# Optimization experiments

Hardware: AMD Instinct MI355X
Metric: run time of the kernel (lower is better)

## Reference

```python
import jax, jax.numpy as jnp
import numpy as np

B_, L_, DM, DS, DC, EX = 4, 2048, 1024, 16, 4, 2
DI = DM * EX

def setup_inputs() -> dict:
    key = jax.random.key(0)
    ks = jax.random.split(key, 8)
    s = lambda i, shape, scale: jax.random.normal(ks[i], shape, jnp.float32) * scale
    return dict(
        x=s(0, (B_, L_, DM), 1.0),
        in_proj_w=s(1, (2 * DI, DM), 0.02),
        conv_weight=s(2, (DI, DC), 0.1),
        conv_bias=jnp.zeros((DI,), jnp.float32),
        A_log=jax.random.uniform(ks[3], (DS,), jnp.float32, -4.0, -1.0),
        D=jnp.ones((DI,), jnp.float32),
        delta_w=s(4, (DS, DI), 0.02),
        delta_b=jnp.ones((DS,), jnp.float32),
        B_w=s(5, (DS, DI), 0.02),
        C_w=s(6, (DS, DI), 0.02),
        out_proj_w=s(7, (DM, DI), 0.02),
    )

def reference(x, in_proj_w, conv_weight, conv_bias, A_log, D, delta_w, delta_b, B_w, C_w, out_proj_w):
    Bb, L, Dm = x.shape
    di, dc = conv_weight.shape
    # 1. input projection and split into ssm / gate branches
    x_inner = x @ in_proj_w.T                       # [B,L,2*di]
    x_ssm, x_gate = x_inner[..., :di], x_inner[..., di:]
    # 2. causal depthwise conv1d + SiLU (kernel size dc, per-channel weights)
    xp = jnp.pad(x_ssm, ((0, 0), (dc - 1, 0), (0, 0)))
    xc = conv_bias + sum(xp[:, k:k + L, :] * conv_weight[:, k] for k in range(dc))
    x_conv = jax.nn.silu(xc)                         # [B,L,di]
    # 3. content-aware discretization
    delta = jax.nn.softplus(x_conv @ delta_w.T + delta_b)  # [B,L,N]
    Bs = x_conv @ B_w.T                              # [B,L,N]
    Cs = x_conv @ C_w.T                              # [B,L,N]
    A = -jnp.exp(A_log)                              # [N]
    xavg = x_conv.mean(axis=-1)                      # [B,L]
    # 4. selective SSM scan over L with state h:[B,N]
    def step(h, inp):
        dt, bt, ct, xa = inp                         # [B,N],[B,N],[B,N],[B]
        h = jnp.exp(dt * A) * h + dt * bt * xa[:, None]
        return h, (h * ct).sum(-1)                   # y_t: [B]
    h0 = jnp.zeros((Bb, A.shape[0]), x.dtype)
    _, ys = jax.lax.scan(
        step, h0,
        (delta.transpose(1, 0, 2), Bs.transpose(1, 0, 2), Cs.transpose(1, 0, 2), xavg.T))
    y_ssm = ys.T[..., None]                          # [B,L,1] (broadcasts over di)
    # 5. gate, skip, output projection
    y_gated = y_ssm * jax.nn.silu(x_gate)
    y_skip = y_gated + x_conv * D
    return y_skip @ out_proj_w.T                     # [B,L,D]
```

## Files before the change

### kernel.cpp

```cpp
#include <hip/hip_runtime.h>
#include <cmath>

#define LL 2048
#define NROW 8192
#define DMODEL 1024
#define DINNER 2048
#define NSTATE 16
#define NSEG 64
#define SEGLEN 32

typedef unsigned short u16;
typedef __attribute__((ext_vector_type(8))) unsigned short u16x8;
typedef __attribute__((ext_vector_type(8))) short short8;
typedef __attribute__((ext_vector_type(4))) float floatx4;
typedef __attribute__((ext_vector_type(16))) float floatx16;

__device__ __forceinline__ float bf2f(u16 h) {
    unsigned u = ((unsigned)h) << 16;
    float f;
    __builtin_memcpy(&f, &u, 4);
    return f;
}
__device__ __forceinline__ u16 f2bf(float f) {
    unsigned u;
    __builtin_memcpy(&u, &f, 4);
    u = u + 0x7fffu + ((u >> 16) & 1u);
    return (u16)(u >> 16);
}
__device__ __forceinline__ float silu_f(float x) { return x / (1.f + __expf(-x)); }

__global__ __launch_bounds__(256) void cvt_multi(
    const float* __restrict__ s0, const float* __restrict__ s1,
    const float* __restrict__ s2, const float* __restrict__ s3,
    const float* __restrict__ s4, const float* __restrict__ s5,
    u16* __restrict__ d0, u16* __restrict__ d1, u16* __restrict__ d2,
    u16* __restrict__ d3, u16* __restrict__ d4, u16* __restrict__ d5) {
    int bid = blockIdx.x;
    const float* s;
    u16* d;
    size_t off;
    if (bid < 4096)      { s = s0; d = d0; off = (size_t)bid * 2048; }
    else if (bid < 6144) { s = s1; d = d1; off = (size_t)(bid - 4096) * 2048; }
    else if (bid < 7168) { s = s2; d = d2; off = (size_t)(bid - 6144) * 2048; }
    else if (bid < 7184) { s = s3; d = d3; off = (size_t)(bid - 7168) * 2048; }
    else if (bid < 7200) { s = s4; d = d4; off = (size_t)(bid - 7184) * 2048; }
    else                 { s = s5; d = d5; off = (size_t)(bid - 7200) * 2048; }
    size_t i = off + (size_t)threadIdx.x * 8;
    float4 a = *(const float4*)&s[i];
    float4 b = *(const float4*)&s[i + 4];
    u16x8 o;
    o[0] = f2bf(a.x); o[1] = f2bf(a.y); o[2] = f2bf(a.z); o[3] = f2bf(a.w);
    o[4] = f2bf(b.x); o[5] = f2bf(b.y); o[6] = f2bf(b.z); o[7] = f2bf(b.w);
    *(u16x8*)&d[i] = o;
}

#define GL_LDS(gp, lp)                                                        \
    __builtin_amdgcn_global_load_lds(                                         \
        (const __attribute__((address_space(1))) void*)(gp),                  \
        (__attribute__((address_space(3))) void*)(lp), 16, 0, 0)

template <int OUT_BF16>
__global__ __launch_bounds__(512, 2) void gemm_bt_256(
    const u16* __restrict__ A, const u16* __restrict__ B,
    void* __restrict__ Cout, int N, int K) {
    __shared__ u16 sA[2][2][256 * 32];
    __shared__ u16 sB[2][2][256 * 32];
    const int tid = threadIdx.x;
    const int lane = tid & 63;
    const int wave = tid >> 6;
    const int wm = wave >> 2;
    const int wn = wave & 3;
    const int bm = blockIdx.y * 256;
    const int bn = blockIdx.x * 256;

    const int srow = lane >> 2;
    const int kbg = (lane & 3) ^ ((lane >> 3) & 3);
    const u16* aBase[2];
    const u16* bBase[2];
#pragma unroll
    for (int p = 0; p < 2; ++p) {
        int chunk = wave * 2 + p;
        aBase[p] = A + (size_t)(bm + chunk * 16 + srow) * K + kbg * 8;
        bBase[p] = B + (size_t)(bn + chunk * 16 + srow) * K + kbg * 8;
    }
    const int ldsOff0 = (wave * 2) * 512;
    const int ldsOff1 = (wave * 2 + 1) * 512;

#define STAGE_A(buf, kh, kt)                                                  \
    do {                                                                      \
        GL_LDS(aBase[0] + (kt) * 64 + (kh) * 32, &sA[buf][kh][ldsOff0]);      \
        GL_LDS(aBase[1] + (kt) * 64 + (kh) * 32, &sA[buf][kh][ldsOff1]);      \
    } while (0)
#define STAGE_B(buf, kh, kt)                                                  \
    do {                                                                      \
        GL_LDS(bBase[0] + (kt) * 64 + (kh) * 32, &sB[buf][kh][ldsOff0]);      \
        GL_LDS(bBase[1] + (kt) * 64 + (kh) * 32, &sB[buf][kh][ldsOff1]);      \
    } while (0)

    const int fr = lane & 15;
    const int kq = lane >> 4;
    const int ks2 = kq ^ ((fr >> 1) & 3);
    int aoff[2][4], boff[4];
#pragma unroll
    for (int qm = 0; qm < 2; ++qm)
#pragma unroll
        for (int mi = 0; mi < 4; ++mi)
            aoff[qm][mi] = (wm * 128 + qm * 64 + mi * 16 + fr) * 32 + ks2 * 8;
#pragma unroll
    for (int ni = 0; ni < 4; ++ni)
        boff[ni] = (wn * 64 + ni * 16 + fr) * 32 + ks2 * 8;

#define READ_A(dst, qm, kh, buf)                                              \
    do {                                                                      \
        _Pragma("unroll")                                                     \
        for (int mi = 0; mi < 4; ++mi)                                        \
            dst[mi] = *(const short8*)&sA[buf][kh][aoff[qm][mi]];             \
    } while (0)
#define READ_B(dst, kh, buf)                                                  \
    do {                                                                      \
        _Pragma("unroll")                                                     \
        for (int ni = 0; ni < 4; ++ni)                                        \
            dst[ni] = *(const short8*)&sB[buf][kh][boff[ni]];                 \
    } while (0)
#define MFMA16(base, AF, BF)                                                  \
    do {                                                                      \
        _Pragma("unroll")                                                     \
        for (int mi = 0; mi < 4; ++mi)                                        \
            _Pragma("unroll")                                                 \
            for (int ni = 0; ni < 4; ++ni)                                    \
                acc[(base) + mi][ni] = __builtin_amdgcn_mfma_f32_16x16x32_bf16( \
                    AF[mi], BF[ni], acc[(base) + mi][ni], 0, 0, 0);           \
    } while (0)

    floatx4 acc[8][4];
#pragma unroll
    for (int i = 0; i < 8; ++i)
#pragma unroll
        for (int j = 0; j < 4; ++j) acc[i][j] = (floatx4){0.f, 0.f, 0.f, 0.f};

    short8 afA[4], afB[4], bfA[4], bfB[4];

    STAGE_A(0, 0, 0);
    STAGE_B(0, 0, 0);
    STAGE_A(0, 1, 0);
    STAGE_B(0, 1, 0);
    asm volatile("s_waitcnt vmcnt(0)" ::: "memory");
    __builtin_amdgcn_s_barrier();
    READ_A(afA, 0, 0, 0);
    READ_B(bfA, 0, 0);
    __builtin_amdgcn_sched_barrier(0);

    const int NT = K >> 6;
    for (int t = 0; t < NT; ++t) {
        const int cur = t & 1;
        const int nxt = cur ^ 1;
        int tn = t + 1;
        if (tn == NT) tn = 0;

        asm volatile("s_waitcnt lgkmcnt(0)" ::: "memory");
        __builtin_amdgcn_sched_barrier(0);
        READ_A(afB, 1, 0, cur);
        STAGE_A(nxt, 0, tn);
        __builtin_amdgcn_sched_barrier(0);
        __builtin_amdgcn_s_setprio(1);
        MFMA16(0, afA, bfA);
        __builtin_amdgcn_s_setprio(0);

        asm volatile("s_waitcnt lgkmcnt(0)" ::: "memory");
        __builtin_amdgcn_sched_barrier(0);
        asm volatile("s_waitcnt vmcnt(2)" ::: "memory");
        __builtin_amdgcn_s_barrier();
        READ_A(afA, 0, 1, cur);
        READ_B(bfB, 1, cur);
        STAGE_B(nxt, 0, tn);
        __builtin_amdgcn_sched_barrier(0);
        __builtin_amdgcn_s_setprio(1);
        MFMA16(4, afB, bfA);
        __builtin_amdgcn_s_setprio(0);

        asm volatile("s_waitcnt lgkmcnt(0)" ::: "memory");
        __builtin_amdgcn_sched_barrier(0);
        READ_A(afB, 1, 1, cur);
        STAGE_A(nxt, 1, tn);
        __builtin_amdgcn_sched_barrier(0);
        __builtin_amdgcn_s_setprio(1);
        MFMA16(0, afA, bfB);
        __builtin_amdgcn_s_setprio(0);

        asm volatile("s_waitcnt lgkmcnt(0)" ::: "memory");
        __builtin_amdgcn_sched_barrier(0);
        asm volatile("s_waitcnt vmcnt(2)" ::: "memory");
        __builtin_amdgcn_s_barrier();
        READ_A(afA, 0, 0, nxt);
        READ_B(bfA, 0, nxt);
        STAGE_B(nxt, 1, tn);
        __builtin_amdgcn_sched_barrier(0);
        __builtin_amdgcn_s_setprio(1);
        MFMA16(4, afB, bfB);
        __builtin_amdgcn_s_setprio(0);
    }

    const int cc = lane & 15;
    const int rb = (lane >> 4) * 4;
#pragma unroll
    for (int mi = 0; mi < 8; ++mi)
#pragma unroll
        for (int ni = 0; ni < 4; ++ni)
#pragma unroll
            for (int r = 0; r < 4; ++r) {
                int grow = bm + wm * 128 + mi * 16 + rb + r;
                int gcol = bn + wn * 64 + ni * 16 + cc;
                float v = acc[mi][ni][r];
                if (OUT_BF16)
                    ((u16*)Cout)[(size_t)grow * N + gcol] = f2bf(v);
                else
                    ((float*)Cout)[(size_t)grow * N + gcol] = v;
            }
#undef STAGE_A
#undef STAGE_B
#undef READ_A
#undef READ_B
#undef MFMA16
}

template <int OUT_BF16>
__global__ __launch_bounds__(256) void gemm_bt_mfma(
    const u16* __restrict__ A, const u16* __restrict__ B,
    void* __restrict__ Cout, int N, int K) {
    __shared__ u16 As[128 * 32];
    __shared__ u16 Bs[128 * 32];
    const int tid = threadIdx.x;
    const int lane = tid & 63;
    const int wave = tid >> 6;
    const int bm = blockIdx.y * 128;
    const int bn = blockIdx.x * 128;

    const int kbg = (lane & 3) ^ ((lane >> 3) & 3);
    const int srow = lane >> 2;
    const u16* ag[2];
    const u16* bg[2];
#pragma unroll
    for (int p = 0; p < 2; ++p) {
        int c = wave * 2 + p;
        ag[p] = A + (size_t)(bm + c * 16 + srow) * K + kbg * 8;
        bg[p] = B + (size_t)(bn + c * 16 + srow) * K + kbg * 8;
    }
    const int frow = lane & 31;
    const int khi = lane >> 5;
    const int wr = (wave >> 1) * 64;
    const int wc = (wave & 1) * 64;
    int aoff[2][2], boff[2][2];
#pragma unroll
    for (int mi = 0; mi < 2; ++mi)
#pragma unroll
        for (int kh = 0; kh < 2; ++kh) {
            int rA = wr + mi * 32 + frow;
            int rB = wc + mi * 32 + frow;
            int kb = kh * 2 + khi;
            aoff[mi][kh] = rA * 32 + (kb ^ ((rA >> 1) & 3)) * 8;
            boff[mi][kh] = rB * 32 + (kb ^ ((rB >> 1) & 3)) * 8;
        }
    floatx16 acc[2][2];
#pragma unroll
    for (int i = 0; i < 2; ++i)
#pragma unroll
        for (int j = 0; j < 2; ++j) acc[i][j] = (floatx16)(0.f);

    for (int k0 = 0; k0 < K; k0 += 32) {
        __syncthreads();
#pragma unroll
        for (int p = 0; p < 2; ++p) {
            int c = wave * 2 + p;
            __builtin_amdgcn_global_load_lds(
                (const __attribute__((address_space(1))) void*)ag[p],
                (__attribute__((address_space(3))) void*)&As[c * 512], 16, 0, 0);
            __builtin_amdgcn_global_load_lds(
                (const __attribute__((address_space(1))) void*)bg[p],
                (__attribute__((address_space(3))) void*)&Bs[c * 512], 16, 0, 0);
            ag[p] += 32;
            bg[p] += 32;
        }
        __syncthreads();
        short8 af[2][2], bf[2][2];
#pragma unroll
        for (int mi = 0; mi < 2; ++mi)
#pragma unroll
            for (int kh = 0; kh < 2; ++kh) {
                af[mi][kh] = *(const short8*)&As[aoff[mi][kh]];
                bf[mi][kh] = *(const short8*)&Bs[boff[mi][kh]];
            }
#pragma unroll
        for (int kh = 0; kh < 2; ++kh)
#pragma unroll
            for (int mi = 0; mi < 2; ++mi)
#pragma unroll
                for (int ni = 0; ni < 2; ++ni)
                    acc[mi][ni] = __builtin_amdgcn_mfma_f32_32x32x16_bf16(
                        af[mi][kh], bf[ni][kh], acc[mi][ni], 0, 0, 0);
    }
    const int cc = lane & 31;
    const int rbase = 4 * (lane >> 5);
#pragma unroll
    for (int mi = 0; mi < 2; ++mi)
#pragma unroll
        for (int ni = 0; ni < 2; ++ni)
#pragma unroll
            for (int r = 0; r < 16; ++r) {
                int grow = bm + wr + mi * 32 + (r & 3) + 8 * (r >> 2) + rbase;
                int gcol = bn + wc + ni * 32 + cc;
                float v = acc[mi][ni][r];
                if (OUT_BF16)
                    ((u16*)Cout)[(size_t)grow * N + gcol] = f2bf(v);
                else
                    ((float*)Cout)[(size_t)grow * N + gcol] = v;
            }
}

__global__ __launch_bounds__(256) void conv_silu_avg(
    const u16* __restrict__ xin, const float* __restrict__ cw,
    const float* __restrict__ cb, u16* __restrict__ xconv,
    float* __restrict__ xavg) {
    const int blk = blockIdx.x;
    const int b = blk >> 7;
    const int lc = blk & 127;
    const int row0 = b * LL + lc * 16;
    const int tid = threadIdx.x;
    const int lane = tid & 63, wave = tid >> 6;
    const int d0 = tid * 8;
    float4 cwv[8];
    float cbv[8];
#pragma unroll
    for (int e = 0; e < 8; ++e) cwv[e] = *(const float4*)&cw[(d0 + e) * 4];
#pragma unroll
    for (int e = 0; e < 8; e += 4) {
        float4 c = *(const float4*)&cb[d0 + e];
        cbv[e] = c.x; cbv[e + 1] = c.y; cbv[e + 2] = c.z; cbv[e + 3] = c.w;
    }
    u16x8 w0, w1, w2;
    if (lc == 0) {
        w0 = (u16x8)0; w1 = (u16x8)0; w2 = (u16x8)0;
    } else {
        w0 = *(const u16x8*)&xin[(size_t)(row0 - 3) * (2 * DINNER) + d0];
        w1 = *(const u16x8*)&xin[(size_t)(row0 - 2) * (2 * DINNER) + d0];
        w2 = *(const u16x8*)&xin[(size_t)(row0 - 1) * (2 * DINNER) + d0];
    }
    float sums[16];
#pragma unroll
    for (int t = 0; t < 16; ++t) {
        u16x8 cur = *(const u16x8*)&xin[(size_t)(row0 + t) * (2 * DINNER) + d0];
        float lsum = 0.f;
        u16x8 o;
#pragma unroll
        for (int e = 0; e < 8; ++e) {
            float acc = cbv[e];
            acc += bf2f(w0[e]) * cwv[e].x;
            acc += bf2f(w1[e]) * cwv[e].y;
            acc += bf2f(w2[e]) * cwv[e].z;
            acc += bf2f(cur[e]) * cwv[e].w;
            float s = silu_f(acc);
            lsum += s;
            o[e] = f2bf(s);
        }
        *(u16x8*)&xconv[(size_t)(row0 + t) * DINNER + d0] = o;
        sums[t] = lsum;
        w0 = w1; w1 = w2; w2 = cur;
    }
#pragma unroll
    for (int off = 32; off; off >>= 1)
#pragma unroll
        for (int t = 0; t < 16; ++t) sums[t] += __shfl_down(sums[t], off);
    __shared__ float wred[4][16];
    if (lane == 0) {
#pragma unroll
        for (int t = 0; t < 16; ++t) wred[wave][t] = sums[t];
    }
    __syncthreads();
    if (tid < 16)
        xavg[row0 + tid] = (wred[0][tid] + wred[1][tid] + wred[2][tid] + wred[3][tid]) *
                           (1.f / DINNER);
}

__global__ __launch_bounds__(256) void dbc_direct(
    const u16* __restrict__ xconv, const u16* __restrict__ wcat,
    const float* __restrict__ db, const float* __restrict__ A_log,
    const float* __restrict__ xavg,
    float* __restrict__ a_out, float* __restrict__ u_out, float* __restrict__ c_out) {
    __shared__ float part[4][32][48];
    const int tid = threadIdx.x;
    const int lane = tid & 63;
    const int wave = tid >> 6;
    const int bm = blockIdx.x * 32;
    const int fr = lane & 15;
    const int kq = lane >> 4;
    const int k0 = wave * 512 + kq * 8;

    const u16* ap0 = xconv + (size_t)(bm + fr) * DINNER + k0;
    const u16* ap1 = xconv + (size_t)(bm + 16 + fr) * DINNER + k0;
    const u16* bp0 = wcat + (size_t)(fr) * DINNER + k0;
    const u16* bp1 = wcat + (size_t)(16 + fr) * DINNER + k0;
    const u16* bp2 = wcat + (size_t)(32 + fr) * DINNER + k0;

    floatx4 acc[2][3];
#pragma unroll
    for (int mi = 0; mi < 2; ++mi)
#pragma unroll
        for (int ni = 0; ni < 3; ++ni) acc[mi][ni] = (floatx4){0.f, 0.f, 0.f, 0.f};

#pragma unroll 4
    for (int kk = 0; kk < 16; ++kk) {
        short8 a0 = *(const short8*)ap0;
        short8 a1 = *(const short8*)ap1;
        short8 b0 = *(const short8*)bp0;
        short8 b1 = *(const short8*)bp1;
        short8 b2 = *(const short8*)bp2;
        ap0 += 32; ap1 += 32; bp0 += 32; bp1 += 32; bp2 += 32;
        acc[0][0] = __builtin_amdgcn_mfma_f32_16x16x32_bf16(a0, b0, acc[0][0], 0, 0, 0);
        acc[0][1] = __builtin_amdgcn_mfma_f32_16x16x32_bf16(a0, b1, acc[0][1], 0, 0, 0);
        acc[0][2] = __builtin_amdgcn_mfma_f32_16x16x32_bf16(a0, b2, acc[0][2], 0, 0, 0);
        acc[1][0] = __builtin_amdgcn_mfma_f32_16x16x32_bf16(a1, b0, acc[1][0], 0, 0, 0);
        acc[1][1] = __builtin_amdgcn_mfma_f32_16x16x32_bf16(a1, b1, acc[1][1], 0, 0, 0);
        acc[1][2] = __builtin_amdgcn_mfma_f32_16x16x32_bf16(a1, b2, acc[1][2], 0, 0, 0);
    }
    const int cr = kq * 4;
#pragma unroll
    for (int mi = 0; mi < 2; ++mi)
#pragma unroll
        for (int ni = 0; ni < 3; ++ni)
#pragma unroll
            for (int r = 0; r < 4; ++r)
                part[wave][mi * 16 + cr + r][ni * 16 + fr] = acc[mi][ni][r];
    __syncthreads();
#pragma unroll
    for (int it = tid; it < 512; it += 256) {
        int row = it >> 4;
        int s = it & 15;
        float sd = 0.f, sb = 0.f, sc = 0.f;
#pragma unroll
        for (int w = 0; w < 4; ++w) {
            sd += part[w][row][s];
            sb += part[w][row][s + 16];
            sc += part[w][row][s + 32];
        }
        int grow = bm + row;
        float Aa = -__expf(A_log[s]);
        float pre = sd + db[s];
        float delta = (pre > 20.f) ? pre : log1pf(__expf(pre));
        a_out[grow * NSTATE + s] = __expf(delta * Aa);
        u_out[grow * NSTATE + s] = delta * sb * xavg[grow];
        c_out[grow * NSTATE + s] = sc;
    }
}

__global__ __launch_bounds__(256) void scan_p1(
    const float* __restrict__ a, const float* __restrict__ u,
    float* __restrict__ Pc, float* __restrict__ H0c) {
    int gid = blockIdx.x * 256 + threadIdx.x;
    int s = gid & 15, seg = (gid >> 4) & (NSEG - 1), b = gid >> 10;
    size_t base = (size_t)(b * LL + seg * SEGLEN) * NSTATE + s;
    float P = 1.f, h = 0.f;
#pragma unroll 8
    for (int t = 0; t < SEGLEN; ++t) {
        float av = a[base + (size_t)t * NSTATE];
        float uv = u[base + (size_t)t * NSTATE];
        h = fmaf(av, h, uv);
        P *= av;
    }
    int o = (b * NSEG + seg) * NSTATE + s;
    Pc[o] = P;
    H0c[o] = h;
}

__global__ __launch_bounds__(64) void scan_p2(
    const float* __restrict__ Pc, const float* __restrict__ H0c,
    float* __restrict__ hstart) {
    int lane = threadIdx.x;
    int b = lane >> 4, s = lane & 15;
    float h = 0.f;
#pragma unroll 8
    for (int seg = 0; seg < NSEG; ++seg) {
        int o = (b * NSEG + seg) * NSTATE + s;
        hstart[o] = h;
        h = fmaf(Pc[o], h, H0c[o]);
    }
}

__global__ __launch_bounds__(256) void scan_p3(
    const float* __restrict__ a, const float* __restrict__ u,
    const float* __restrict__ c, const float* __restrict__ hstart,
    float* __restrict__ y) {
    int gid = blockIdx.x * 256 + threadIdx.x;
    int s = gid & 15, seg = (gid >> 4) & (NSEG - 1), b = gid >> 10;
    float h = hstart[(b * NSEG + seg) * NSTATE + s];
    size_t base = (size_t)(b * LL + seg * SEGLEN) * NSTATE + s;
#pragma unroll 8
    for (int t = 0; t < SEGLEN; ++t) {
        float av = a[base + (size_t)t * NSTATE];
        float uv = u[base + (size_t)t * NSTATE];
        float cv = c[base + (size_t)t * NSTATE];
        h = fmaf(av, h, uv);
        float p = h * cv;
        p += __shfl_xor(p, 1);
        p += __shfl_xor(p, 2);
        p += __shfl_xor(p, 4);
        p += __shfl_xor(p, 8);
        if (s == 0) y[b * LL + seg * SEGLEN + t] = p;
    }
}

__global__ __launch_bounds__(256) void gate_skip(
    const u16* __restrict__ xin, const float* __restrict__ y,
    const float* __restrict__ Dv, const u16* __restrict__ xconv,
    u16* __restrict__ yskip) {
    size_t i = ((size_t)blockIdx.x * 256 + threadIdx.x) * 8;
    int row = (int)(i >> 11);
    int d = (int)(i & (DINNER - 1));
    u16x8 g = *(const u16x8*)&xin[(size_t)row * (2 * DINNER) + DINNER + d];
    u16x8 xc = *(const u16x8*)&xconv[i];
    float yv = y[row];
    u16x8 o;
#pragma unroll
    for (int e = 0; e < 8; ++e) {
        float gv = silu_f(bf2f(g[e]));
        float v = yv * gv + bf2f(xc[e]) * Dv[d + e];
        o[e] = f2bf(v);
    }
    *(u16x8*)&yskip[i] = o;
}

extern "C" void kernel_launch(void* const* d_in, const int* in_sizes, int n_in,
                              void* d_out, int out_size, void* d_ws, size_t ws_size,
                              hipStream_t stream) {
    const float* x       = (const float*)d_in[0];
    const float* w_in    = (const float*)d_in[1];
    const float* conv_w  = (const float*)d_in[2];
    const float* conv_b  = (const float*)d_in[3];
    const float* A_log   = (const float*)d_in[4];
    const float* Dv      = (const float*)d_in[5];
    const float* delta_w = (const float*)d_in[6];
    const float* delta_b = (const float*)d_in[7];
    const float* B_w     = (const float*)d_in[8];
    const float* C_w     = (const float*)d_in[9];
    const float* out_w   = (const float*)d_in[10];
    float* out = (float*)d_out;

    u16* xb  = (u16*)d_ws;
    u16* wb  = xb + 8388608;
    u16* owb = wb + 4194304;
    u16* wsb = owb + 2097152;
    u16* xin = wsb + 98304;
    u16* xcv = xin + 33554432;
    u16* ysk = xcv + 16777216;
    float* fb     = (float*)(ysk + 16777216);
    float* abuf   = fb;
    float* ubuf   = abuf + 131072;
    float* cbuf   = ubuf + 131072;
    float* pbuf   = cbuf + 131072;
    float* h0buf  = pbuf + 4096;
    float* hsbuf  = h0buf + 4096;
    float* ybuf   = hsbuf + 4096;
    float* avgbuf = ybuf + 8192;

    cvt_multi<<<7216, 256, 0, stream>>>(x, w_in, out_w, delta_w, B_w, C_w,
                                        xb, wb, owb, wsb, wsb + 32768, wsb + 65536);

    gemm_bt_256<1><<<dim3(16, 32), 512, 0, stream>>>(xb, wb, xin, 2 * DINNER, DMODEL);

    conv_silu_avg<<<512, 256, 0, stream>>>(xin, conv_w, conv_b, xcv, avgbuf);
    dbc_direct<<<256, 256, 0, stream>>>(xcv, wsb, delta_b, A_log, avgbuf,
                                        abuf, ubuf, cbuf);

    scan_p1<<<16, 256, 0, stream>>>(abuf, ubuf, pbuf, h0buf);
    scan_p2<<<1, 64, 0, stream>>>(pbuf, h0buf, hsbuf);
    scan_p3<<<16, 256, 0, stream>>>(abuf, ubuf, cbuf, hsbuf, ybuf);

    gate_skip<<<NROW * DINNER / 8 / 256, 256, 0, stream>>>(xin, ybuf, Dv, xcv, ysk);

    gemm_bt_mfma<0><<<dim3(8, 64), 256, 0, stream>>>(ysk, owb, out, DMODEL, DINNER);
}
```

Measured before the change: 326.0 us.

## Restructure 256x256 GEMM main loop with 64-wide K LDS layout and staggered prefetch

Reorganizes the 256-tile bf16 GEMM so LDS holds full 64-wide K rows in two 128-row halves with an 8-slot XOR swizzle instead of two 32-wide K halves. The main loop becomes four phases per K tile, each reading fragments, issuing a global-to-LDS load and running 16 MFMAs. A prefetches one tile ahead and B two tiles ahead, reusing the current B buffer. The goal is fewer LDS reads per MFMA and more load/compute overlap, at the cost of many more block barriers and a tighter buffer-reuse schedule with more ordering hazards.

```diff
diff --git a/kernel.cpp b/kernel.cpp
--- a/kernel.cpp
+++ b/kernel.cpp
@@ -58,13 +58,20 @@
     __builtin_amdgcn_global_load_lds(                                         \
         (const __attribute__((address_space(1))) void*)(gp),                  \
         (__attribute__((address_space(3))) void*)(lp), 16, 0, 0)
+#define BAR() __builtin_amdgcn_s_barrier()
+#define LGKM0()                                                               \
+    do {                                                                      \
+        asm volatile("s_waitcnt lgkmcnt(0)" ::: "memory");                    \
+        __builtin_amdgcn_sched_barrier(0);                                    \
+    } while (0)
+#define VMC4() asm volatile("s_waitcnt vmcnt(4)" ::: "memory")
 
 template <int OUT_BF16>
 __global__ __launch_bounds__(512, 2) void gemm_bt_256(
     const u16* __restrict__ A, const u16* __restrict__ B,
     void* __restrict__ Cout, int N, int K) {
-    __shared__ u16 sA[2][2][256 * 32];
-    __shared__ u16 sB[2][2][256 * 32];
+    __shared__ u16 sA[2][2][128 * 64];
+    __shared__ u16 sB[2][2][128 * 64];
     const int tid = threadIdx.x;
     const int lane = tid & 63;
     const int wave = tid >> 6;
@@ -73,131 +80,127 @@
     const int bm = blockIdx.y * 256;
     const int bn = blockIdx.x * 256;
 
-    const int srow = lane >> 2;
-    const int kbg = (lane & 3) ^ ((lane >> 3) & 3);
-    const u16* aBase[2];
-    const u16* bBase[2];
-#pragma unroll
-    for (int p = 0; p < 2; ++p) {
-        int chunk = wave * 2 + p;
-        aBase[p] = A + (size_t)(bm + chunk * 16 + srow) * K + kbg * 8;
-        bBase[p] = B + (size_t)(bn + chunk * 16 + srow) * K + kbg * 8;
-    }
-    const int ldsOff0 = (wave * 2) * 512;
-    const int ldsOff1 = (wave * 2 + 1) * 512;
-
-#define STAGE_A(buf, kh, kt)                                                  \
+    const int gslot = (lane & 7) ^ ((lane >> 3) & 7);
+    const int srowoff = lane >> 3;
+    const u16* aG = A + (size_t)(bm + wave * 8 + srowoff) * K + gslot * 8;
+    const u16* bG = B + (size_t)(bn + wave * 8 + srowoff) * K + gslot * 8;
+    const size_t row64 = (size_t)64 * K;
+    const size_t row128 = (size_t)128 * K;
+
+#define STAGE_A(buf, h, kt)                                                   \
     do {                                                                      \
-        GL_LDS(aBase[0] + (kt) * 64 + (kh) * 32, &sA[buf][kh][ldsOff0]);      \
-        GL_LDS(aBase[1] + (kt) * 64 + (kh) * 32, &sA[buf][kh][ldsOff1]);      \
+        const u16* g_ = aG + (h) * row128 + (size_t)(kt) * 64;                \
+        GL_LDS(g_,         &sA[buf][h][wave * 512]);                          \
+        GL_LDS(g_ + row64, &sA[buf][h][(8 + wave) * 512]);                    \
     } while (0)
-#define STAGE_B(buf, kh, kt)                                                  \
+#define STAGE_B(buf, h, kt)                                                   \
     do {                                                                      \
-        GL_LDS(bBase[0] + (kt) * 64 + (kh) * 32, &sB[buf][kh][ldsOff0]);      \
-        GL_LDS(bBase[1] + (kt) * 64 + (kh) * 32, &sB[buf][kh][ldsOff1]);      \
+        const u16* g_ = bG + (h) * row128 + (size_t)(kt) * 64;                \
+        GL_LDS(g_,         &sB[buf][h][wave * 512]);                          \
+        GL_LDS(g_ + row64, &sB[buf][h][(8 + wave) * 512]);                    \
     } while (0)
 
     const int fr = lane & 15;
     const int kq = lane >> 4;
-    const int ks2 = kq ^ ((fr >> 1) & 3);
-    int aoff[2][4], boff[4];
-#pragma unroll
-    for (int qm = 0; qm < 2; ++qm)
-#pragma unroll
-        for (int mi = 0; mi < 4; ++mi)
-            aoff[qm][mi] = (wm * 128 + qm * 64 + mi * 16 + fr) * 32 + ks2 * 8;
-#pragma unroll
-    for (int ni = 0; ni < 4; ++ni)
-        boff[ni] = (wn * 64 + ni * 16 + fr) * 32 + ks2 * 8;
-
-#define READ_A(dst, qm, kh, buf)                                              \
+    const int st0 = kq ^ (fr & 7);
+    const int st1 = (4 + kq) ^ (fr & 7);
+    const int aB0 = fr * 64 + st0 * 8;
+    const int aB1 = fr * 64 + st1 * 8;
+    const int bRow = (wn & 1) * 64 + fr;
+    const int bB0 = bRow * 64 + st0 * 8;
+    const int bB1 = bRow * 64 + st1 * 8;
+
+    floatx4 acc[8][4];
+#pragma unroll
+    for (int i = 0; i < 8; ++i)
+#pragma unroll
+        for (int j = 0; j < 4; ++j) acc[i][j] = (floatx4){0.f, 0.f, 0.f, 0.f};
+
+    short8 af[4][2], bf01[2][2], bf23[2][2];
+
+#define MFMA_PH(mibase, BF, nibase)                                           \
     do {                                                                      \
         _Pragma("unroll")                                                     \
-        for (int mi = 0; mi < 4; ++mi)                                        \
-            dst[mi] = *(const short8*)&sA[buf][kh][aoff[qm][mi]];             \
+        for (int kh = 0; kh < 2; ++kh)                                        \
+            _Pragma("unroll")                                                 \
+            for (int mi = 0; mi < 4; ++mi)                                    \
+                _Pragma("unroll")                                             \
+                for (int ni = 0; ni < 2; ++ni)                                \
+                    acc[(mibase) + mi][(nibase) + ni] =                       \
+                        __builtin_amdgcn_mfma_f32_16x16x32_bf16(              \
+                            af[mi][kh], BF[ni][kh],                           \
+                            acc[(mibase) + mi][(nibase) + ni], 0, 0, 0);      \
     } while (0)
-#define READ_B(dst, kh, buf)                                                  \
-    do {                                                                      \
-        _Pragma("unroll")                                                     \
-        for (int ni = 0; ni < 4; ++ni)                                        \
-            dst[ni] = *(const short8*)&sB[buf][kh][boff[ni]];                 \
-    } while (0)
-#define MFMA16(base, AF, BF)                                                  \
-    do {                                                                      \
-        _Pragma("unroll")                                                     \
-        for (int mi = 0; mi < 4; ++mi)                                        \
-            _Pragma("unroll")                                                 \
-            for (int ni = 0; ni < 4; ++ni)                                    \
-                acc[(base) + mi][ni] = __builtin_amdgcn_mfma_f32_16x16x32_bf16( \
-                    AF[mi], BF[ni], acc[(base) + mi][ni], 0, 0, 0);           \
-    } while (0)
-
-    floatx4 acc[8][4];
-#pragma unroll
-    for (int i = 0; i < 8; ++i)
-#pragma unroll
-        for (int j = 0; j < 4; ++j) acc[i][j] = (floatx4){0.f, 0.f, 0.f, 0.f};
-
-    short8 afA[4], afB[4], bfA[4], bfB[4];
 
     STAGE_A(0, 0, 0);
+    STAGE_A(0, 1, 0);
     STAGE_B(0, 0, 0);
-    STAGE_A(0, 1, 0);
     STAGE_B(0, 1, 0);
-    asm volatile("s_waitcnt vmcnt(0)" ::: "memory");
-    __builtin_amdgcn_s_barrier();
-    READ_A(afA, 0, 0, 0);
-    READ_B(bfA, 0, 0);
-    __builtin_amdgcn_sched_barrier(0);
+    STAGE_B(1, 0, 1);
+    STAGE_B(1, 1, 1);
+    VMC4();
+    BAR();
 
     const int NT = K >> 6;
     for (int t = 0; t < NT; ++t) {
         const int cur = t & 1;
         const int nxt = cur ^ 1;
-        int tn = t + 1;
-        if (tn == NT) tn = 0;
-
-        asm volatile("s_waitcnt lgkmcnt(0)" ::: "memory");
-        __builtin_amdgcn_sched_barrier(0);
-        READ_A(afB, 1, 0, cur);
-        STAGE_A(nxt, 0, tn);
-        __builtin_amdgcn_sched_barrier(0);
+        const int kA = (t + 1) & (NT - 1);
+        const int kB = (t + 2) & (NT - 1);
+        const u16* aC = &sA[cur][wm][0];
+        const u16* bC = &sB[cur][wn >> 1][0];
+
+#pragma unroll
+        for (int mi = 0; mi < 4; ++mi) {
+            af[mi][0] = *(const short8*)(aC + aB0 + mi * 16 * 64);
+            af[mi][1] = *(const short8*)(aC + aB1 + mi * 16 * 64);
+        }
+#pragma unroll
+        for (int ni = 0; ni < 2; ++ni) {
+            bf01[ni][0] = *(const short8*)(bC + bB0 + ni * 16 * 64);
+            bf01[ni][1] = *(const short8*)(bC + bB1 + ni * 16 * 64);
+        }
+        STAGE_A(nxt, 0, kA);
+        BAR();
+        LGKM0();
         __builtin_amdgcn_s_setprio(1);
-        MFMA16(0, afA, bfA);
+        MFMA_PH(0, bf01, 0);
         __builtin_amdgcn_s_setprio(0);
-
-        asm volatile("s_waitcnt lgkmcnt(0)" ::: "memory");
-        __builtin_amdgcn_sched_barrier(0);
-        asm volatile("s_waitcnt vmcnt(2)" ::: "memory");
-        __builtin_amdgcn_s_barrier();
-        READ_A(afA, 0, 1, cur);
-        READ_B(bfB, 1, cur);
-        STAGE_B(nxt, 0, tn);
-        __builtin_amdgcn_sched_barrier(0);
+        BAR();
+
+#pragma unroll
+        for (int ni = 0; ni < 2; ++ni) {
+            bf23[ni][0] = *(const short8*)(bC + bB0 + (32 + ni * 16) * 64);
+            bf23[ni][1] = *(const short8*)(bC + bB1 + (32 + ni * 16) * 64);
+        }
+        STAGE_A(nxt, 1, kA);
+        BAR();
+        LGKM0();
         __builtin_amdgcn_s_setprio(1);
-        MFMA16(4, afB, bfA);
+        MFMA_PH(0, bf23, 2);
         __builtin_amdgcn_s_setprio(0);
-
-        asm volatile("s_waitcnt lgkmcnt(0)" ::: "memory");
-        __builtin_amdgcn_sched_barrier(0);
-        READ_A(afB, 1, 1, cur);
-        STAGE_A(nxt, 1, tn);
-        __builtin_amdgcn_sched_barrier(0);
+        BAR();
+
+#pragma unroll
+        for (int mi = 0; mi < 4; ++mi) {
+            af[mi][0] = *(const short8*)(aC + aB0 + (64 + mi * 16) * 64);
+            af[mi][1] = *(const short8*)(aC + aB1 + (64 + mi * 16) * 64);
+        }
+        STAGE_B(cur, 0, kB);
+        BAR();
+        LGKM0();
         __builtin_amdgcn_s_setprio(1);
-        MFMA16(0, afA, bfB);
+        MFMA_PH(4, bf01, 0);
         __builtin_amdgcn_s_setprio(0);
-
-        asm volatile("s_waitcnt lgkmcnt(0)" ::: "memory");
-        __builtin_amdgcn_sched_barrier(0);
-        asm volatile("s_waitcnt vmcnt(2)" ::: "memory");
-        __builtin_amdgcn_s_barrier();
-        READ_A(afA, 0, 0, nxt);
-        READ_B(bfA, 0, nxt);
-        STAGE_B(nxt, 1, tn);
-        __builtin_amdgcn_sched_barrier(0);
+        BAR();
+
+        STAGE_B(cur, 1, kB);
+        BAR();
         __builtin_amdgcn_s_setprio(1);
-        MFMA16(4, afB, bfB);
+        MFMA_PH(4, bf23, 2);
         __builtin_amdgcn_s_setprio(0);
+        VMC4();
+        BAR();
     }
 
     const int cc = lane & 15;
@@ -218,9 +221,7 @@
             }
 #undef STAGE_A
 #undef STAGE_B
-#undef READ_A
-#undef READ_B
-#undef MFMA16
+#undef MFMA_PH
 }
 
 template <int OUT_BF16>
```

Result: faster. 317.3 us (-2.7%).
